# Performance work log

Measured on AMD Instinct MI355X. Metric: run time of the kernel, lower is better.

Reference implementation:

```python
import jax, jax.numpy as jnp
import numpy as np

B, T, D = 32, 4096, 64
K = 512
COMMITMENT_COST = 0.25


def setup_inputs() -> dict:
    key = jax.random.key(0)
    kz, kw = jax.random.split(key)
    z = jax.random.normal(kz, (B, T, D), dtype=jnp.float32)
    # matches nn.init.uniform_(weight, -1/K, 1/K)
    W = jax.random.uniform(kw, (K, D), dtype=jnp.float32, minval=-1.0 / K, maxval=1.0 / K)
    return {"z": z, "W": W}


def reference(z, W):
    b, t, d = z.shape
    z_flat = z.reshape(-1, d)                                   # [N, D]
    # squared euclidean distances via ||z||^2 + ||w||^2 - 2 z.w
    dist = (jnp.sum(z_flat * z_flat, axis=1, keepdims=True)
            + jnp.sum(W * W, axis=1)
            - 2.0 * z_flat @ W.T)                               # [N, K]
    indices = jnp.argmin(dist, axis=1)                          # [N]
    z_q = W[indices].reshape(b, t, d)                           # gather
    # straight-through estimator
    z_q_st = z + jax.lax.stop_gradient(z_q - z)
    loss = COMMITMENT_COST * jnp.mean((z - jax.lax.stop_gradient(z_q_st)) ** 2)
    return z_q_st, indices.reshape(b, t), loss
```

## Files before the change

kernel.cpp:

```cpp
#include <hip/hip_runtime.h>
#include <hip/hip_bf16.h>
#include <math.h>

#define NROWS 131072
#define KC    512
#define DD    64
#define NELEM (NROWS * DD)

#define OUT_IDX_OFF  NELEM
#define OUT_LOSS_OFF (NELEM + NROWS)

#define MARGIN 3e-5f

#define WSO_CNT   0
#define WSO_LOSS  8
#define WSO_DONE  16
#define WSO_WNORM 64
#define WSO_BH    4096
#define WSO_BL    (WSO_BH + 65536)
#define WSO_LIST  (WSO_BL + 65536)

typedef __attribute__((ext_vector_type(8))) short short8;
typedef __attribute__((ext_vector_type(4))) float f32x4;

static __device__ __forceinline__ short f2bf(float f) {
  __hip_bfloat16 h = __float2bfloat16(f);
  short s; __builtin_memcpy(&s, &h, 2); return s;
}
static __device__ __forceinline__ float bf2f(short s) {
  unsigned u = ((unsigned)(unsigned short)s) << 16;
  float f; __builtin_memcpy(&f, &u, 4); return f;
}
static __device__ __forceinline__ void split8(const float* v, short8& hi, short8& lo) {
#pragma unroll
  for (int j = 0; j < 8; j++) {
    float f = v[j];
    short hb = f2bf(f);
    float r = f - bf2f(hb);
    hi[j] = hb;
    lo[j] = f2bf(r);
  }
}

__device__ __forceinline__ float np_sumsq64(const float* __restrict__ p) {
#pragma clang fp contract(off)
  float r0 = p[0] * p[0], r1 = p[1] * p[1], r2 = p[2] * p[2], r3 = p[3] * p[3];
  float r4 = p[4] * p[4], r5 = p[5] * p[5], r6 = p[6] * p[6], r7 = p[7] * p[7];
  for (int i = 8; i < 64; i += 8) {
    r0 = r0 + p[i + 0] * p[i + 0];
    r1 = r1 + p[i + 1] * p[i + 1];
    r2 = r2 + p[i + 2] * p[i + 2];
    r3 = r3 + p[i + 3] * p[i + 3];
    r4 = r4 + p[i + 4] * p[i + 4];
    r5 = r5 + p[i + 5] * p[i + 5];
    r6 = r6 + p[i + 6] * p[i + 6];
    r7 = r7 + p[i + 7] * p[i + 7];
  }
  return ((r0 + r1) + (r2 + r3)) + ((r4 + r5) + (r6 + r7));
}

__global__ void k_prep(const float* __restrict__ W, short8* __restrict__ Bh,
                       short8* __restrict__ Bl, float* __restrict__ wnorm) {
  int gtid = blockIdx.x * blockDim.x + threadIdx.x;
  int t = gtid >> 7, rem = gtid & 127;
  int h = rem >> 6, L = rem & 63;
  int cw = (t << 4) + (L & 15);
  int dbase = (h << 5) + ((L >> 4) << 3);
  const float* p = W + (cw << 6) + dbase;
  float4 u0 = *(const float4*)(p);
  float4 u1 = *(const float4*)(p + 4);
  float v[8] = {u0.x, u0.y, u0.z, u0.w, u1.x, u1.y, u1.z, u1.w};
  short8 hi, lo;
  split8(v, hi, lo);
  Bh[gtid] = hi;
  Bl[gtid] = lo;
  if (gtid < KC) wnorm[gtid] = np_sumsq64(W + (gtid << 6));
}

__global__ __launch_bounds__(256) void k_main(
    const float* __restrict__ z, const float* __restrict__ W,
    const short8* __restrict__ Bh, const short8* __restrict__ Bl,
    const float* __restrict__ wnorm, float* __restrict__ out,
    int* __restrict__ flagList, int* __restrict__ flagCnt,
    float* __restrict__ lossSum) {
  const int lane = threadIdx.x & 63;
  const int wv = threadIdx.x >> 6;
  const int rowBase = blockIdx.x * 128 + wv * 32;
  const int m = lane & 15, quad = lane >> 4;

  short8 Ah[2][2], Al[2][2];
#pragma unroll
  for (int mt = 0; mt < 2; mt++) {
    const float* zp = z + (size_t)(rowBase + (mt << 4) + m) * DD + (quad << 3);
#pragma unroll
    for (int h = 0; h < 2; h++) {
      float4 u0 = *(const float4*)(zp + (h << 5));
      float4 u1 = *(const float4*)(zp + (h << 5) + 4);
      float v[8] = {u0.x, u0.y, u0.z, u0.w, u1.x, u1.y, u1.z, u1.w};
      split8(v, Ah[mt][h], Al[mt][h]);
    }
  }

  float b1[2][4], b2[2][4];
  int bi[2][4];
#pragma unroll
  for (int mt = 0; mt < 2; mt++)
#pragma unroll
    for (int r = 0; r < 4; r++) { b1[mt][r] = 1e30f; b2[mt][r] = 1e30f; bi[mt][r] = 0; }

  for (int t = 0; t < 32; t++) {
    short8 Bhf[2], Blf[2];
#pragma unroll
    for (int h = 0; h < 2; h++) {
      Bhf[h] = Bh[((t * 2 + h) << 6) + lane];
      Blf[h] = Bl[((t * 2 + h) << 6) + lane];
    }
    float wn = wnorm[(t << 4) + m];

    f32x4 acc[2] = {{0.f, 0.f, 0.f, 0.f}, {0.f, 0.f, 0.f, 0.f}};
#pragma unroll
    for (int h = 0; h < 2; h++) {
#pragma unroll
      for (int mt = 0; mt < 2; mt++)
        acc[mt] = __builtin_amdgcn_mfma_f32_16x16x32_bf16(Ah[mt][h], Bhf[h], acc[mt], 0, 0, 0);
#pragma unroll
      for (int mt = 0; mt < 2; mt++)
        acc[mt] = __builtin_amdgcn_mfma_f32_16x16x32_bf16(Al[mt][h], Bhf[h], acc[mt], 0, 0, 0);
#pragma unroll
      for (int mt = 0; mt < 2; mt++)
        acc[mt] = __builtin_amdgcn_mfma_f32_16x16x32_bf16(Ah[mt][h], Blf[h], acc[mt], 0, 0, 0);
    }

    int colv = (t << 4) + m;
#pragma unroll
    for (int mt = 0; mt < 2; mt++)
#pragma unroll
      for (int r = 0; r < 4; r++) {
        float s = fmaf(-2.0f, acc[mt][r], wn);
        if (s < b1[mt][r]) { b2[mt][r] = b1[mt][r]; b1[mt][r] = s; bi[mt][r] = colv; }
        else b2[mt][r] = fminf(b2[mt][r], s);
      }
  }

#pragma unroll
  for (int off = 1; off < 16; off <<= 1) {
#pragma unroll
    for (int mt = 0; mt < 2; mt++)
#pragma unroll
      for (int r = 0; r < 4; r++) {
        float o1 = __shfl_xor(b1[mt][r], off, 64);
        float o2 = __shfl_xor(b2[mt][r], off, 64);
        int oi = __shfl_xor(bi[mt][r], off, 64);
        if (o1 < b1[mt][r] || (o1 == b1[mt][r] && oi < bi[mt][r])) {
          b2[mt][r] = fminf(b1[mt][r], o2);
          b1[mt][r] = o1; bi[mt][r] = oi;
        } else {
          b2[mt][r] = fminf(b2[mt][r], o1);
        }
      }
  }

  float lossAcc = 0.f;
#pragma unroll
  for (int mt = 0; mt < 2; mt++)
#pragma unroll
    for (int lr = 0; lr < 16; lr++) {
      const int q = lr >> 2, r = lr & 3;
      int ki = __shfl(bi[mt][r], q << 4, 64);
      float gap = b2[mt][r] - b1[mt][r];
      float gapr = __shfl(gap, q << 4, 64);
      int row = rowBase + (mt << 4) + lr;
      float zv = z[(size_t)row * DD + lane];
      float w = W[(ki << 6) + lane];
      float tt = w - zv;
      float o = zv + tt;
      out[(size_t)row * DD + lane] = o;
      float dl = zv - o;
      lossAcc = fmaf(dl, dl, lossAcc);
      if (lane == 0) {
        out[OUT_IDX_OFF + row] = (float)ki;
        if (gapr < MARGIN) {
          int slot = atomicAdd(flagCnt, 1);
          flagList[slot] = row;
        }
      }
    }

#pragma unroll
  for (int off = 1; off < 64; off <<= 1) lossAcc += __shfl_xor(lossAcc, off, 64);
  if (lane == 0) atomicAdd(lossSum, lossAcc);
}

__global__ void k_refine(const float* __restrict__ z, const float* __restrict__ W,
                         const float* __restrict__ wnp, float* __restrict__ out,
                         const int* __restrict__ flagList,
                         const int* __restrict__ flagCnt,
                         float* __restrict__ lossSum, int* __restrict__ doneCnt) {
  int nflag = *flagCnt;
  int lane = threadIdx.x & 63;
  int wave = (blockIdx.x * blockDim.x + threadIdx.x) >> 6;
  int nWaves = (gridDim.x * blockDim.x) >> 6;

  for (int f = wave; f < nflag; f += nWaves) {
    int row = flagList[f];
    const float* zr = z + (size_t)row * DD;
    float A = np_sumsq64(zr);

    float best = 1e30f;
    int bk = 0x7fffffff;
#pragma unroll
    for (int j = 0; j < KC / 64; j++) {
      int k = lane + (j << 6);
      const float* wk = W + (k << 6);
      double cd = 0.0;
      for (int d = 0; d < DD; d++) cd = fma((double)zr[d], (double)wk[d], cd);
      float twoC = (float)(2.0 * cd);
      float dist;
      {
#pragma clang fp contract(off)
        float t1 = A + wnp[k];
        dist = t1 - twoC;
      }
      if (dist < best || (dist == best && k < bk)) { best = dist; bk = k; }
    }
#pragma unroll
    for (int off = 1; off < 64; off <<= 1) {
      float ov = __shfl_xor(best, off, 64);
      int ok = __shfl_xor(bk, off, 64);
      if (ov < best || (ov == best && ok < bk)) { best = ov; bk = ok; }
    }

    int kold = (int)out[OUT_IDX_OFF + row];
    if (bk != kold) {
      float zv = zr[lane];
      float wN = W[(bk << 6) + lane];
      float oOld = out[(size_t)row * DD + lane];
      float tN = wN - zv;
      float oN = zv + tN;
      out[(size_t)row * DD + lane] = oN;
      float dN = zv - oN, dO = zv - oOld;
      float delta = dN * dN - dO * dO;
#pragma unroll
      for (int off = 1; off < 64; off <<= 1) delta += __shfl_xor(delta, off, 64);
      if (lane == 0) {
        atomicAdd(lossSum, delta);
        out[OUT_IDX_OFF + row] = (float)bk;
      }
    }
  }

  __syncthreads();
  if (threadIdx.x == 0) {
    __threadfence();
    int old = atomicAdd(doneCnt, 1);
    if (old == (int)gridDim.x - 1) {
      __threadfence();
      float ls = atomicAdd(lossSum, 0.0f);
      out[OUT_LOSS_OFF] = 0.25f * ls / (float)NELEM;
    }
  }
}

extern "C" void kernel_launch(void* const* d_in, const int* in_sizes, int n_in,
                              void* d_out, int out_size, void* d_ws, size_t ws_size,
                              hipStream_t stream) {
  const float* z = (const float*)d_in[0];
  const float* W = (const float*)d_in[1];
  float* out = (float*)d_out;
  char* ws = (char*)d_ws;

  int* flagCnt = (int*)(ws + WSO_CNT);
  float* lossSum = (float*)(ws + WSO_LOSS);
  int* doneCnt = (int*)(ws + WSO_DONE);
  float* wnorm = (float*)(ws + WSO_WNORM);
  short8* Bh = (short8*)(ws + WSO_BH);
  short8* Bl = (short8*)(ws + WSO_BL);
  int* flagList = (int*)(ws + WSO_LIST);

  hipMemsetAsync(d_ws, 0, 64, stream);

  k_prep<<<16, 256, 0, stream>>>(W, Bh, Bl, wnorm);
  k_main<<<NROWS / 128, 256, 0, stream>>>(z, W, Bh, Bl, wnorm, out,
                                          flagList, flagCnt, lossSum);
  k_refine<<<256, 256, 0, stream>>>(z, W, wnorm, out, flagList, flagCnt,
                                    lossSum, doneCnt);
}
```

Before: 208.7 us.

## Stage codebook fragments through double-buffered LDS with register prefetch

Instead of every wave reading the bf16 hi/lo codebook fragments and norms straight from global memory on each tile, the block now cooperatively loads chunks of four tiles into LDS. It prefetches the next chunk into registers while computing on the current one, using a ping-pong buffer with a barrier per chunk. Launch bounds now also ask for 4 blocks per multiprocessor. The aim is to cut redundant global/L2 traffic and hide load latency, at the cost of about 33KB of LDS per block, extra registers and block-wide syncs that could limit occupancy.

```diff
diff --git a/kernel.cpp b/kernel.cpp
--- a/kernel.cpp
+++ b/kernel.cpp
@@ -77,16 +77,19 @@
   if (gtid < KC) wnorm[gtid] = np_sumsq64(W + (gtid << 6));
 }
 
-__global__ __launch_bounds__(256) void k_main(
+__global__ __launch_bounds__(256, 4) void k_main(
     const float* __restrict__ z, const float* __restrict__ W,
     const short8* __restrict__ Bh, const short8* __restrict__ Bl,
     const float* __restrict__ wnorm, float* __restrict__ out,
     int* __restrict__ flagList, int* __restrict__ flagCnt,
     float* __restrict__ lossSum) {
-  const int lane = threadIdx.x & 63;
-  const int wv = threadIdx.x >> 6;
+  const int tid = threadIdx.x;
+  const int lane = tid & 63;
+  const int wv = tid >> 6;
   const int rowBase = blockIdx.x * 128 + wv * 32;
   const int m = lane & 15, quad = lane >> 4;
+
+  __shared__ float4 ldsBuf[2080];
 
   short8 Ah[2][2], Al[2][2];
 #pragma unroll
@@ -108,38 +111,71 @@
 #pragma unroll
     for (int r = 0; r < 4; r++) { b1[mt][r] = 1e30f; b2[mt][r] = 1e30f; bi[mt][r] = 0; }
 
-  for (int t = 0; t < 32; t++) {
-    short8 Bhf[2], Blf[2];
-#pragma unroll
-    for (int h = 0; h < 2; h++) {
-      Bhf[h] = Bh[((t * 2 + h) << 6) + lane];
-      Blf[h] = Bl[((t * 2 + h) << 6) + lane];
-    }
-    float wn = wnorm[(t << 4) + m];
-
-    f32x4 acc[2] = {{0.f, 0.f, 0.f, 0.f}, {0.f, 0.f, 0.f, 0.f}};
-#pragma unroll
-    for (int h = 0; h < 2; h++) {
+  const float4* gBh = (const float4*)Bh;
+  const float4* gBl = (const float4*)Bl;
+  const float4* gWn = (const float4*)wnorm;
+
+  float4 nr0, nr1, nr2, nr3, nr4;
+  nr0 = gBh[tid];        nr1 = gBh[tid + 256];
+  nr2 = gBl[tid];        nr3 = gBl[tid + 256];
+  if (tid < 16) nr4 = gWn[tid];
+  ldsBuf[tid] = nr0;        ldsBuf[tid + 256] = nr1;
+  ldsBuf[512 + tid] = nr2;  ldsBuf[512 + tid + 256] = nr3;
+  if (tid < 16) ldsBuf[1024 + tid] = nr4;
+  __syncthreads();
+
+  for (int c = 0; c < 8; c++) {
+    const int b = c & 1;
+    if (c < 7) {
+      const int g = (c + 1) << 9;
+      nr0 = gBh[g + tid];        nr1 = gBh[g + tid + 256];
+      nr2 = gBl[g + tid];        nr3 = gBl[g + tid + 256];
+      if (tid < 16) nr4 = gWn[((c + 1) << 4) + tid];
+    }
+
+    const float4* L = ldsBuf + b * 1040;
+#pragma unroll
+    for (int tc = 0; tc < 4; tc++) {
+      short8 Bhf[2], Blf[2];
+#pragma unroll
+      for (int h = 0; h < 2; h++) {
+        Bhf[h] = *(const short8*)&L[((tc * 2 + h) << 6) + lane];
+        Blf[h] = *(const short8*)&L[512 + ((tc * 2 + h) << 6) + lane];
+      }
+      float wn = ((const float*)&L[1024])[(tc << 4) + m];
+
+      f32x4 acc[2] = {{0.f, 0.f, 0.f, 0.f}, {0.f, 0.f, 0.f, 0.f}};
+#pragma unroll
+      for (int h = 0; h < 2; h++) {
+#pragma unroll
+        for (int mt = 0; mt < 2; mt++)
+          acc[mt] = __builtin_amdgcn_mfma_f32_16x16x32_bf16(Ah[mt][h], Bhf[h], acc[mt], 0, 0, 0);
+#pragma unroll
+        for (int mt = 0; mt < 2; mt++)
+          acc[mt] = __builtin_amdgcn_mfma_f32_16x16x32_bf16(Al[mt][h], Bhf[h], acc[mt], 0, 0, 0);
+#pragma unroll
+        for (int mt = 0; mt < 2; mt++)
+          acc[mt] = __builtin_amdgcn_mfma_f32_16x16x32_bf16(Ah[mt][h], Blf[h], acc[mt], 0, 0, 0);
+      }
+
+      int colv = (((c << 2) + tc) << 4) + m;
 #pragma unroll
       for (int mt = 0; mt < 2; mt++)
-        acc[mt] = __builtin_amdgcn_mfma_f32_16x16x32_bf16(Ah[mt][h], Bhf[h], acc[mt], 0, 0, 0);
-#pragma unroll
-      for (int mt = 0; mt < 2; mt++)
-        acc[mt] = __builtin_amdgcn_mfma_f32_16x16x32_bf16(Al[mt][h], Bhf[h], acc[mt], 0, 0, 0);
-#pragma unroll
-      for (int mt = 0; mt < 2; mt++)
-        acc[mt] = __builtin_amdgcn_mfma_f32_16x16x32_bf16(Ah[mt][h], Blf[h], acc[mt], 0, 0, 0);
-    }
-
-    int colv = (t << 4) + m;
-#pragma unroll
-    for (int mt = 0; mt < 2; mt++)
-#pragma unroll
-      for (int r = 0; r < 4; r++) {
-        float s = fmaf(-2.0f, acc[mt][r], wn);
-        if (s < b1[mt][r]) { b2[mt][r] = b1[mt][r]; b1[mt][r] = s; bi[mt][r] = colv; }
-        else b2[mt][r] = fminf(b2[mt][r], s);
-      }
+#pragma unroll
+        for (int r = 0; r < 4; r++) {
+          float s = fmaf(-2.0f, acc[mt][r], wn);
+          if (s < b1[mt][r]) { b2[mt][r] = b1[mt][r]; b1[mt][r] = s; bi[mt][r] = colv; }
+          else b2[mt][r] = fminf(b2[mt][r], s);
+        }
+    }
+
+    if (c < 7) {
+      float4* Ld = ldsBuf + (1 - b) * 1040;
+      Ld[tid] = nr0;        Ld[tid + 256] = nr1;
+      Ld[512 + tid] = nr2;  Ld[512 + tid + 256] = nr3;
+      if (tid < 16) Ld[1024 + tid] = nr4;
+    }
+    __syncthreads();
   }
 
 #pragma unroll
```

New measurement: 203.0 us. -2.8%, faster.

## Stage codebook fragments in double-buffered LDS and halve rows per wave

Applied to the files above, without the earlier changes.

The main kernel now cooperatively copies the split bf16 codebook fragments from global memory into a double-buffered shared-memory tile. The next chunk is prefetched into registers while the current chunk is consumed by MFMA. Each wave now handles 16 rows instead of 32, doubling the grid, and launch bounds request 2 blocks per CU. The aim is to cut redundant per-wave global reads of the codebook and raise occupancy, at the cost of block-wide barriers each chunk and halving codebook reuse per fragment load.

```diff
diff --git a/kernel.cpp b/kernel.cpp
--- a/kernel.cpp
+++ b/kernel.cpp
@@ -77,114 +77,132 @@
   if (gtid < KC) wnorm[gtid] = np_sumsq64(W + (gtid << 6));
 }
 
-__global__ __launch_bounds__(256) void k_main(
+__global__ __launch_bounds__(256, 2) void k_main(
     const float* __restrict__ z, const float* __restrict__ W,
     const short8* __restrict__ Bh, const short8* __restrict__ Bl,
     const float* __restrict__ wnorm, float* __restrict__ out,
     int* __restrict__ flagList, int* __restrict__ flagCnt,
     float* __restrict__ lossSum) {
-  const int lane = threadIdx.x & 63;
-  const int wv = threadIdx.x >> 6;
-  const int rowBase = blockIdx.x * 128 + wv * 32;
+  const int tid = threadIdx.x;
+  const int lane = tid & 63;
+  const int wv = tid >> 6;
+  const int rowBase = blockIdx.x * 64 + wv * 16;
   const int m = lane & 15, quad = lane >> 4;
 
-  short8 Ah[2][2], Al[2][2];
-#pragma unroll
-  for (int mt = 0; mt < 2; mt++) {
-    const float* zp = z + (size_t)(rowBase + (mt << 4) + m) * DD + (quad << 3);
+  __shared__ float4 ldsBuf[2048];
+
+  short8 Ah[2], Al[2];
+  {
+    const float* zp = z + (size_t)(rowBase + m) * DD + (quad << 3);
 #pragma unroll
     for (int h = 0; h < 2; h++) {
       float4 u0 = *(const float4*)(zp + (h << 5));
       float4 u1 = *(const float4*)(zp + (h << 5) + 4);
       float v[8] = {u0.x, u0.y, u0.z, u0.w, u1.x, u1.y, u1.z, u1.w};
-      split8(v, Ah[mt][h], Al[mt][h]);
-    }
-  }
-
-  float b1[2][4], b2[2][4];
-  int bi[2][4];
-#pragma unroll
-  for (int mt = 0; mt < 2; mt++)
-#pragma unroll
-    for (int r = 0; r < 4; r++) { b1[mt][r] = 1e30f; b2[mt][r] = 1e30f; bi[mt][r] = 0; }
-
-  for (int t = 0; t < 32; t++) {
-    short8 Bhf[2], Blf[2];
-#pragma unroll
-    for (int h = 0; h < 2; h++) {
-      Bhf[h] = Bh[((t * 2 + h) << 6) + lane];
-      Blf[h] = Bl[((t * 2 + h) << 6) + lane];
-    }
-    float wn = wnorm[(t << 4) + m];
-
-    f32x4 acc[2] = {{0.f, 0.f, 0.f, 0.f}, {0.f, 0.f, 0.f, 0.f}};
-#pragma unroll
-    for (int h = 0; h < 2; h++) {
-#pragma unroll
-      for (int mt = 0; mt < 2; mt++)
-        acc[mt] = __builtin_amdgcn_mfma_f32_16x16x32_bf16(Ah[mt][h], Bhf[h], acc[mt], 0, 0, 0);
-#pragma unroll
-      for (int mt = 0; mt < 2; mt++)
-        acc[mt] = __builtin_amdgcn_mfma_f32_16x16x32_bf16(Al[mt][h], Bhf[h], acc[mt], 0, 0, 0);
-#pragma unroll
-      for (int mt = 0; mt < 2; mt++)
-        acc[mt] = __builtin_amdgcn_mfma_f32_16x16x32_bf16(Ah[mt][h], Blf[h], acc[mt], 0, 0, 0);
-    }
-
-    int colv = (t << 4) + m;
-#pragma unroll
-    for (int mt = 0; mt < 2; mt++)
+      split8(v, Ah[h], Al[h]);
+    }
+  }
+
+  float b1[4], b2[4];
+  int bi[4];
+#pragma unroll
+  for (int r = 0; r < 4; r++) { b1[r] = 1e30f; b2[r] = 1e30f; bi[r] = 0; }
+
+  const float4* gBh = (const float4*)Bh;
+  const float4* gBl = (const float4*)Bl;
+
+  {
+    float4 s0 = gBh[tid], s1 = gBh[256 + tid];
+    float4 s2 = gBl[tid], s3 = gBl[256 + tid];
+    ldsBuf[tid] = s0;        ldsBuf[256 + tid] = s1;
+    ldsBuf[512 + tid] = s2;  ldsBuf[768 + tid] = s3;
+  }
+  __syncthreads();
+
+  for (int c = 0; c < 8; c++) {
+    const int b = c & 1;
+    float4 s0, s1, s2, s3;
+    if (c < 7) {
+      const int g = (c + 1) << 9;
+      s0 = gBh[g + tid];       s1 = gBh[g + 256 + tid];
+      s2 = gBl[g + tid];       s3 = gBl[g + 256 + tid];
+    }
+    float wn4[4];
+#pragma unroll
+    for (int tc = 0; tc < 4; tc++) wn4[tc] = wnorm[((((c << 2) + tc)) << 4) + m];
+
+    const float4* L = ldsBuf + (b << 10);
+#pragma unroll
+    for (int tc = 0; tc < 4; tc++) {
+      short8 Bhf0 = *(const short8*)&L[((tc << 1) << 6) + lane];
+      short8 Bhf1 = *(const short8*)&L[(((tc << 1) + 1) << 6) + lane];
+      short8 Blf0 = *(const short8*)&L[512 + ((tc << 1) << 6) + lane];
+      short8 Blf1 = *(const short8*)&L[512 + (((tc << 1) + 1) << 6) + lane];
+
+      f32x4 acc = {0.f, 0.f, 0.f, 0.f};
+      acc = __builtin_amdgcn_mfma_f32_16x16x32_bf16(Ah[0], Bhf0, acc, 0, 0, 0);
+      acc = __builtin_amdgcn_mfma_f32_16x16x32_bf16(Al[0], Bhf0, acc, 0, 0, 0);
+      acc = __builtin_amdgcn_mfma_f32_16x16x32_bf16(Ah[0], Blf0, acc, 0, 0, 0);
+      acc = __builtin_amdgcn_mfma_f32_16x16x32_bf16(Ah[1], Bhf1, acc, 0, 0, 0);
+      acc = __builtin_amdgcn_mfma_f32_16x16x32_bf16(Al[1], Bhf1, acc, 0, 0, 0);
+      acc = __builtin_amdgcn_mfma_f32_16x16x32_bf16(Ah[1], Blf1, acc, 0, 0, 0);
+
+      int colv = ((((c << 2) + tc)) << 4) + m;
 #pragma unroll
       for (int r = 0; r < 4; r++) {
-        float s = fmaf(-2.0f, acc[mt][r], wn);
-        if (s < b1[mt][r]) { b2[mt][r] = b1[mt][r]; b1[mt][r] = s; bi[mt][r] = colv; }
-        else b2[mt][r] = fminf(b2[mt][r], s);
-      }
+        float s = fmaf(-2.0f, acc[r], wn4[tc]);
+        if (s < b1[r]) { b2[r] = b1[r]; b1[r] = s; bi[r] = colv; }
+        else b2[r] = fminf(b2[r], s);
+      }
+    }
+
+    if (c < 7) {
+      float4* Ld = ldsBuf + ((1 - b) << 10);
+      Ld[tid] = s0;        Ld[256 + tid] = s1;
+      Ld[512 + tid] = s2;  Ld[768 + tid] = s3;
+    }
+    __syncthreads();
   }
 
 #pragma unroll
   for (int off = 1; off < 16; off <<= 1) {
 #pragma unroll
-    for (int mt = 0; mt < 2; mt++)
-#pragma unroll
-      for (int r = 0; r < 4; r++) {
-        float o1 = __shfl_xor(b1[mt][r], off, 64);
-        float o2 = __shfl_xor(b2[mt][r], off, 64);
-        int oi = __shfl_xor(bi[mt][r], off, 64);
-        if (o1 < b1[mt][r] || (o1 == b1[mt][r] && oi < bi[mt][r])) {
-          b2[mt][r] = fminf(b1[mt][r], o2);
-          b1[mt][r] = o1; bi[mt][r] = oi;
-        } else {
-          b2[mt][r] = fminf(b2[mt][r], o1);
-        }
-      }
+    for (int r = 0; r < 4; r++) {
+      float o1 = __shfl_xor(b1[r], off, 64);
+      float o2 = __shfl_xor(b2[r], off, 64);
+      int oi = __shfl_xor(bi[r], off, 64);
+      if (o1 < b1[r] || (o1 == b1[r] && oi < bi[r])) {
+        b2[r] = fminf(b1[r], o2);
+        b1[r] = o1; bi[r] = oi;
+      } else {
+        b2[r] = fminf(b2[r], o1);
+      }
+    }
   }
 
   float lossAcc = 0.f;
 #pragma unroll
-  for (int mt = 0; mt < 2; mt++)
-#pragma unroll
-    for (int lr = 0; lr < 16; lr++) {
-      const int q = lr >> 2, r = lr & 3;
-      int ki = __shfl(bi[mt][r], q << 4, 64);
-      float gap = b2[mt][r] - b1[mt][r];
-      float gapr = __shfl(gap, q << 4, 64);
-      int row = rowBase + (mt << 4) + lr;
-      float zv = z[(size_t)row * DD + lane];
-      float w = W[(ki << 6) + lane];
-      float tt = w - zv;
-      float o = zv + tt;
-      out[(size_t)row * DD + lane] = o;
-      float dl = zv - o;
-      lossAcc = fmaf(dl, dl, lossAcc);
-      if (lane == 0) {
-        out[OUT_IDX_OFF + row] = (float)ki;
-        if (gapr < MARGIN) {
-          int slot = atomicAdd(flagCnt, 1);
-          flagList[slot] = row;
-        }
-      }
-    }
+  for (int lr = 0; lr < 16; lr++) {
+    const int q = lr >> 2, r = lr & 3;
+    int ki = __shfl(bi[r], q << 4, 64);
+    float gap = b2[r] - b1[r];
+    float gapr = __shfl(gap, q << 4, 64);
+    int row = rowBase + lr;
+    float zv = z[(size_t)row * DD + lane];
+    float w = W[(ki << 6) + lane];
+    float tt = w - zv;
+    float o = zv + tt;
+    out[(size_t)row * DD + lane] = o;
+    float dl = zv - o;
+    lossAcc = fmaf(dl, dl, lossAcc);
+    if (lane == 0) {
+      out[OUT_IDX_OFF + row] = (float)ki;
+      if (gapr < MARGIN) {
+        int slot = atomicAdd(flagCnt, 1);
+        flagList[slot] = row;
+      }
+    }
+  }
 
 #pragma unroll
   for (int off = 1; off < 64; off <<= 1) lossAcc += __shfl_xor(lossAcc, off, 64);
@@ -280,8 +298,8 @@
   hipMemsetAsync(d_ws, 0, 64, stream);
 
   k_prep<<<16, 256, 0, stream>>>(W, Bh, Bl, wnorm);
-  k_main<<<NROWS / 128, 256, 0, stream>>>(z, W, Bh, Bl, wnorm, out,
-                                          flagList, flagCnt, lossSum);
+  k_main<<<NROWS / 64, 256, 0, stream>>>(z, W, Bh, Bl, wnorm, out,
+                                         flagList, flagCnt, lossSum);
   k_refine<<<256, 256, 0, stream>>>(z, W, wnorm, out, flagList, flagCnt,
                                     lossSum, doneCnt);
 }
```

Result: slower. 302.6 us (+45.0%).
